# Optimization experiments

Hardware: AMD Instinct MI355X
Metric: run time of the kernel (lower is better)

## Reference

```python
import jax, jax.numpy as jnp
import numpy as np

N_HEADS = 16
ALIBI_BIAS_MAX = 8


def _alibi_bias(n_heads, seq_len):
    # MPT build_alibi_bias: bias[h, j] = -(seq_len-1-j) * slope_h, arranged [1,H,1,S]
    pos = jnp.arange(1 - seq_len, 1, dtype=jnp.float32).reshape(1, 1, 1, seq_len)
    m = jnp.arange(1, n_heads + 1, dtype=jnp.float32) * (ALIBI_BIAS_MAX / n_heads)
    slopes = (1.0 / jnp.exp2(m)).reshape(1, n_heads, 1, 1)
    return pos * slopes  # [1,H,1,S]


def setup_inputs() -> dict:
    key = jax.random.key(0)
    k1, k2, k3 = jax.random.split(key, 3)
    B, S, D = 1, 2048, 2048
    x = jax.random.normal(k1, (B, S, D), dtype=jnp.float32)
    # Wqkv: Linear(D, 3D, bias=False); out_proj: Linear(D, D, bias=False)
    w_qkv = jax.random.normal(k2, (3 * D, D), dtype=jnp.float32) * (1.0 / np.sqrt(D))
    w_out = jax.random.normal(k3, (D, D), dtype=jnp.float32) * (1.0 / np.sqrt(D))
    return {"x": x, "w_qkv": w_qkv, "w_out": w_out}


def reference(x, w_qkv, w_out):
    B, S, D = x.shape
    H = N_HEADS
    d = D // H
    qkv = x @ w_qkv.T                              # [B,S,3D]
    q, k, v = jnp.split(qkv, 3, axis=-1)
    q = q.reshape(B, S, H, d).transpose(0, 2, 1, 3)  # [B,H,S,d]
    k = k.reshape(B, S, H, d).transpose(0, 2, 1, 3)
    v = v.reshape(B, S, H, d).transpose(0, 2, 1, 3)
    scale = 1.0 / np.sqrt(d)
    scores = jnp.einsum('bhqd,bhkd->bhqk', q, k) * scale  # [B,H,S,S]
    scores = scores + _alibi_bias(H, S)
    min_val = jnp.finfo(scores.dtype).min
    causal = jnp.tril(jnp.ones((S, S), dtype=bool))
    scores = jnp.where(causal[None, None, :, :], scores, min_val)
    probs = jax.nn.softmax(scores.astype(jnp.float32), axis=-1).astype(q.dtype)
    out = jnp.einsum('bhqk,bhkd->bhqd', probs, v)  # [B,H,S,d]
    out = out.transpose(0, 2, 1, 3).reshape(B, S, D)
    return out @ w_out.T
```

## Files before the change

kernel.cpp:

```cpp
#include <hip/hip_runtime.h>

typedef __bf16 bf16;
typedef __bf16 bf16x8 __attribute__((ext_vector_type(8)));
typedef __bf16 bf16x4 __attribute__((ext_vector_type(4)));
typedef float f32x4 __attribute__((ext_vector_type(4)));

#if __has_builtin(__builtin_amdgcn_exp2f)
#define EXP2(x) __builtin_amdgcn_exp2f(x)
#else
#define EXP2(x) exp2f(x)
#endif

__device__ __forceinline__ void gload_lds16(const void* g, void* l) {
  __builtin_amdgcn_global_load_lds(
      (const __attribute__((address_space(1))) void*)g,
      (__attribute__((address_space(3))) void*)l, 16, 0, 0);
}

__global__ __launch_bounds__(256) void cast_all(const float* __restrict__ x,
                                                const float* __restrict__ wqkv,
                                                const float* __restrict__ wout,
                                                bf16* __restrict__ x_bf,
                                                bf16* __restrict__ wqkv_bf,
                                                bf16* __restrict__ wout_bf) {
  const int b = blockIdx.x;
  const float* src;
  bf16* dst;
  int i;
  if (b < 4096) {
    src = x; dst = x_bf; i = b * 1024 + threadIdx.x * 4;
  } else if (b < 16384) {
    src = wqkv; dst = wqkv_bf; i = (b - 4096) * 1024 + threadIdx.x * 4;
  } else {
    src = wout; dst = wout_bf; i = (b - 16384) * 1024 + threadIdx.x * 4;
  }
  float4 v = *(const float4*)(src + i);
  bf16x4 o = {(bf16)v.x, (bf16)v.y, (bf16)v.z, (bf16)v.w};
  *(bf16x4*)(dst + i) = o;
}

__global__ __launch_bounds__(512, 6) void gemm1_qkv(const bf16* __restrict__ A,
                                                    const bf16* __restrict__ B,
                                                    bf16* __restrict__ qb,
                                                    bf16* __restrict__ kb,
                                                    bf16* __restrict__ vt) {
  constexpr int K = 2048;
  __shared__ bf16 As[128 * 32];
  __shared__ bf16 Bs[128 * 32];
  const int t = threadIdx.x;
  const int w = t >> 6, l = t & 63;
  const int lr = l & 15, lg = l >> 4;
  const int nwg = 768;
  int lin = blockIdx.y * 48 + blockIdx.x;
  lin = (lin & 7) * (nwg >> 3) + (lin >> 3);
  const int bn = lin % 48;
  const int bm = lin / 48;
  const int wr = w >> 2, wc = w & 3;

  f32x4 acc[4][2] = {};
  const int row0 = t >> 2;
  const int cc0 = (t & 3) * 8;

  for (int k0 = 0; k0 < K; k0 += 32) {
    gload_lds16(A + (size_t)(bm * 128 + row0) * K + k0 + cc0, (char*)As + w * 1024);
    gload_lds16(B + (size_t)(bn * 128 + row0) * K + k0 + cc0, (char*)Bs + w * 1024);
    __syncthreads();
    bf16x8 af[4], bfr[2];
#pragma unroll
    for (int i = 0; i < 4; ++i)
      af[i] = *(const bf16x8*)((const char*)As + (wr * 64 + i * 16 + lr) * 64 + lg * 16);
#pragma unroll
    for (int j = 0; j < 2; ++j)
      bfr[j] = *(const bf16x8*)((const char*)Bs + (wc * 32 + j * 16 + lr) * 64 + lg * 16);
#pragma unroll
    for (int mi = 0; mi < 4; ++mi)
#pragma unroll
      for (int ni = 0; ni < 2; ++ni)
        acc[mi][ni] = __builtin_amdgcn_mfma_f32_16x16x32_bf16(af[mi], bfr[ni],
                                                              acc[mi][ni], 0, 0, 0);
    __syncthreads();
  }

  const int mb = bm * 128 + wr * 64 + lg * 4;
  const int nb = bn * 128 + wc * 32 + lr;
  if (bn * 128 < 4096) {
    bf16* dst = (bn * 128 < 2048) ? qb : kb;
#pragma unroll
    for (int mi = 0; mi < 4; ++mi) {
      const int mg = mb + mi * 16;
#pragma unroll
      for (int ni = 0; ni < 2; ++ni) {
        const int ng = (nb + ni * 16) & 2047;
#pragma unroll
        for (int rr = 0; rr < 4; ++rr)
          dst[(size_t)(mg + rr) * 2048 + ng] = (bf16)acc[mi][ni][rr];
      }
    }
  } else {
#pragma unroll
    for (int mi = 0; mi < 4; ++mi) {
      const int mg = mb + mi * 16;
#pragma unroll
      for (int ni = 0; ni < 2; ++ni) {
        const int dc = nb + ni * 16 - 4096;
        bf16x4 pk = {(bf16)acc[mi][ni][0], (bf16)acc[mi][ni][1],
                     (bf16)acc[mi][ni][2], (bf16)acc[mi][ni][3]};
        *(bf16x4*)(vt + (size_t)dc * 2048 + mg) = pk;
      }
    }
  }
}

__global__ __launch_bounds__(256) void gemm2_64x128(const bf16* __restrict__ A,
                                                    const bf16* __restrict__ B,
                                                    float* __restrict__ Cf) {
  constexpr int K = 2048, N = 2048;
  __shared__ bf16 As[64 * 32];
  __shared__ bf16 Bs[128 * 32];
  const int t = threadIdx.x;
  const int w = t >> 6, l = t & 63;
  const int lr = l & 15, lg = l >> 4;
  int lin = blockIdx.y * 16 + blockIdx.x;
  lin = (lin & 7) * 64 + (lin >> 3);
  const int bn = lin % 16;
  const int bm = lin / 16;

  f32x4 acc[4][2] = {};

  for (int k0 = 0; k0 < K; k0 += 32) {
    {
      const int row = t >> 2;
      gload_lds16(A + (size_t)(bm * 64 + row) * K + k0 + (t & 3) * 8,
                  (char*)As + (w * 64) * 16);
    }
#pragma unroll
    for (int r = 0; r < 2; ++r) {
      const int c = r * 256 + t;
      const int row = c >> 2;
      gload_lds16(B + (size_t)(bn * 128 + row) * K + k0 + (c & 3) * 8,
                  (char*)Bs + (r * 256 + w * 64) * 16);
    }
    __syncthreads();
    bf16x8 af[4], bfr[2];
#pragma unroll
    for (int i = 0; i < 4; ++i)
      af[i] = *(const bf16x8*)((const char*)As + (i * 16 + lr) * 64 + lg * 16);
#pragma unroll
    for (int i = 0; i < 2; ++i)
      bfr[i] = *(const bf16x8*)((const char*)Bs + (w * 32 + i * 16 + lr) * 64 + lg * 16);
#pragma unroll
    for (int mi = 0; mi < 4; ++mi)
#pragma unroll
      for (int ni = 0; ni < 2; ++ni)
        acc[mi][ni] = __builtin_amdgcn_mfma_f32_16x16x32_bf16(af[mi], bfr[ni],
                                                              acc[mi][ni], 0, 0, 0);
    __syncthreads();
  }

  const int mb = bm * 64 + lg * 4;
  const int nb = bn * 128 + w * 32 + lr;
#pragma unroll
  for (int mi = 0; mi < 4; ++mi) {
    const int mg = mb + mi * 16;
#pragma unroll
    for (int ni = 0; ni < 2; ++ni) {
      const int ng = nb + ni * 16;
#pragma unroll
      for (int rr = 0; rr < 4; ++rr)
        Cf[(size_t)(mg + rr) * N + ng] = acc[mi][ni][rr];
    }
  }
}

__global__ __launch_bounds__(256) void attn_kernel(const bf16* __restrict__ qb,
                                                   const bf16* __restrict__ kb,
                                                   const bf16* __restrict__ vt,
                                                   bf16* __restrict__ out,
                                                   bf16* __restrict__ pA,
                                                   bf16* __restrict__ pB,
                                                   float* __restrict__ ml) {
  constexpr int S = 2048, D = 2048;
  __shared__ bf16 Ks[64 * 128];
  __shared__ bf16 Vs[128 * 64];
  __shared__ bf16 Ps[4][16 * 64];
  const int t = threadIdx.x;
  const int w = t >> 6, l = t & 63;
  const int lr = l & 15, lg = l >> 4;
  const int b = blockIdx.x;

  int h, qt, piece, ns;
  if (b < 1024) {
    const int j = b >> 2;
    h = j & 15; qt = 16 + (j >> 4); piece = b & 3; ns = 4;
  } else if (b < 1280) {
    const int j = (b - 1024) >> 1;
    h = j & 15; qt = 8 + (j >> 4); piece = (b - 1024) & 1; ns = 2;
  } else {
    const int i = b - 1280;
    h = i & 15; qt = i >> 4; piece = 0; ns = 1;
  }
  const bool split = (ns > 1);
  const int q0 = qt * 64;
  const float slope2 = exp2f(-0.5f * (float)(h + 1)) * 1.4426950408889634f;
  const float scale2 = 0.08838834764831845f * 1.4426950408889634f;
  const int W = (int)(24.0f / slope2);
  const int s0 = (q0 > W) ? ((q0 - W) >> 6) : 0;
  const int len = qt + 1 - s0;
  const int start = s0 + (len * piece) / ns;
  const int end = s0 + (len * (piece + 1)) / ns;

  bf16x8 qf[4];
  {
    const bf16* qrow = qb + (size_t)(q0 + w * 16 + lr) * D + h * 128 + lg * 8;
#pragma unroll
    for (int kk = 0; kk < 4; ++kk) qf[kk] = *(const bf16x8*)(qrow + kk * 32);
  }

  f32x4 ob[8] = {};
  float mrow[4] = {-1e30f, -1e30f, -1e30f, -1e30f};
  float lrow[4] = {0.f, 0.f, 0.f, 0.f};

  auto stage = [&](int kv0) {
#pragma unroll
    for (int r = 0; r < 4; ++r) {
      {
        const int krow = r * 16 + (t >> 4);
        const int kcc = t & 15;
        gload_lds16(kb + (size_t)(kv0 + krow) * D + h * 128 + ((kcc ^ (krow & 7)) * 8),
                    (char*)Ks + (r * 256 + w * 64) * 16);
      }
      {
        const int vrow = r * 32 + (t >> 3);
        const int vcc = t & 7;
        gload_lds16(vt + (size_t)(h * 128 + vrow) * S + kv0 + ((vcc ^ (vrow & 7)) * 8),
                    (char*)Vs + (r * 256 + w * 64) * 16);
      }
    }
  };

  for (int tile = start; tile < end; ++tile) {
    const int kv0 = tile << 6;
    stage(kv0);
    __syncthreads();

    f32x4 sc[4] = {};
    __builtin_amdgcn_s_setprio(1);
#pragma unroll
    for (int jb = 0; jb < 4; ++jb) {
      const int row = jb * 16 + lr;
#pragma unroll
      for (int kk = 0; kk < 4; ++kk) {
        const int byte = row * 256 + ((kk * 64 + lg * 16) ^ ((row & 7) << 4));
        bf16x8 kf = *(const bf16x8*)((const char*)Ks + byte);
        sc[jb] = __builtin_amdgcn_mfma_f32_16x16x32_bf16(qf[kk], kf, sc[jb], 0, 0, 0);
      }
    }
    __builtin_amdgcn_s_setprio(0);

    float bias[4];
#pragma unroll
    for (int jb = 0; jb < 4; ++jb)
      bias[jb] = slope2 * (float)(kv0 + jb * 16 + lr - (S - 1));
    const bool diag = (tile == qt);
    float xv[4][4], m2r[4];
#pragma unroll
    for (int rr = 0; rr < 4; ++rr) {
#pragma unroll
      for (int jb = 0; jb < 4; ++jb) {
        float v = fmaf(sc[jb][rr], scale2, bias[jb]);
        if (diag && (jb * 16 + lr > w * 16 + lg * 4 + rr)) v = -1e30f;
        xv[rr][jb] = v;
      }
      float m2 = fmaxf(fmaxf(xv[rr][0], xv[rr][1]), fmaxf(xv[rr][2], xv[rr][3]));
      m2 = fmaxf(m2, __shfl_xor(m2, 1));
      m2 = fmaxf(m2, __shfl_xor(m2, 2));
      m2 = fmaxf(m2, __shfl_xor(m2, 4));
      m2 = fmaxf(m2, __shfl_xor(m2, 8));
      m2r[rr] = m2;
    }
    float need = fmaxf(fmaxf(m2r[0] - mrow[0], m2r[1] - mrow[1]),
                       fmaxf(m2r[2] - mrow[2], m2r[3] - mrow[3]));
    if (!__all(need <= 8.0f)) {
#pragma unroll
      for (int rr = 0; rr < 4; ++rr) {
        const float mnew = fmaxf(mrow[rr], m2r[rr]);
        const float cf = EXP2(mrow[rr] - mnew);
        lrow[rr] *= cf;
        mrow[rr] = mnew;
#pragma unroll
        for (int db = 0; db < 8; ++db) ob[db][rr] *= cf;
      }
    }
    char* pbase = (char*)Ps[w];
#pragma unroll
    for (int rr = 0; rr < 4; ++rr) {
      const int prow = lg * 4 + rr;
      const int sw = (prow & 7) << 4;
      float ps = 0.f;
#pragma unroll
      for (int jb = 0; jb < 4; ++jb) {
        const float p = EXP2(xv[rr][jb] - mrow[rr]);
        *(bf16*)(pbase + ((prow * 128 + jb * 32 + lr * 2) ^ sw)) = (bf16)p;
        ps += p;
      }
      lrow[rr] += ps;
    }

    bf16x8 pf[2];
#pragma unroll
    for (int s = 0; s < 2; ++s)
      pf[s] = *(const bf16x8*)(pbase + ((lr * 128 + s * 64 + lg * 16) ^ ((lr & 7) << 4)));
    __builtin_amdgcn_s_setprio(1);
#pragma unroll
    for (int db = 0; db < 8; ++db) {
      const int vrow = db * 16 + lr;
#pragma unroll
      for (int s = 0; s < 2; ++s) {
        const int byte = vrow * 128 + ((s * 64 + lg * 16) ^ ((vrow & 7) << 4));
        bf16x8 vf = *(const bf16x8*)((const char*)Vs + byte);
        ob[db] = __builtin_amdgcn_mfma_f32_16x16x32_bf16(pf[s], vf, ob[db], 0, 0, 0);
      }
    }
    __builtin_amdgcn_s_setprio(0);
    __syncthreads();
  }

  if (!split) {
#pragma unroll
    for (int rr = 0; rr < 4; ++rr) {
      float ls = lrow[rr];
      ls += __shfl_xor(ls, 1);
      ls += __shfl_xor(ls, 2);
      ls += __shfl_xor(ls, 4);
      ls += __shfl_xor(ls, 8);
      const float inv = 1.0f / ls;
      const int mg = q0 + w * 16 + lg * 4 + rr;
#pragma unroll
      for (int db = 0; db < 8; ++db)
        out[(size_t)mg * D + h * 128 + db * 16 + lr] = (bf16)(ob[db][rr] * inv);
    }
  } else {
    bf16* po = (b < 1024) ? pA + (size_t)b * 8192 : pB + (size_t)(b - 1024) * 8192;
#pragma unroll
    for (int rr = 0; rr < 4; ++rr) {
      float ls = lrow[rr];
      ls += __shfl_xor(ls, 1);
      ls += __shfl_xor(ls, 2);
      ls += __shfl_xor(ls, 4);
      ls += __shfl_xor(ls, 8);
      const int row = w * 16 + lg * 4 + rr;
#pragma unroll
      for (int db = 0; db < 8; ++db)
        po[row * 128 + db * 16 + lr] = (bf16)ob[db][rr];
      if (lr == 0) {
        ml[b * 128 + row] = mrow[rr];
        ml[b * 128 + 64 + row] = ls;
      }
    }
  }
}

__global__ __launch_bounds__(256) void attn_merge(const bf16* __restrict__ pA,
                                                  const bf16* __restrict__ pB,
                                                  const float* __restrict__ ml,
                                                  bf16* __restrict__ out) {
  const int j = blockIdx.x;
  const int t = threadIdx.x;
  int ns, c0, h, qt;
  if (j < 256) {
    ns = 4; c0 = 4 * j; h = j & 15; qt = 16 + (j >> 4);
  } else {
    const int j2 = j - 256;
    ns = 2; c0 = 1024 + 2 * j2; h = j2 & 15; qt = 8 + (j2 >> 4);
  }
  const int q0 = qt * 64;
  const int row = t >> 2;
  const int col0 = (t & 3) * 32;

  float m[4], lv[4];
  float M = -1e30f;
  for (int i = 0; i < ns; ++i) {
    m[i] = ml[(c0 + i) * 128 + row];
    lv[i] = ml[(c0 + i) * 128 + 64 + row];
    M = fmaxf(M, m[i]);
  }
  float wsum = 0.f, wgt[4];
  for (int i = 0; i < ns; ++i) {
    wgt[i] = EXP2(m[i] - M);
    wsum += wgt[i] * lv[i];
  }
  const float inv = 1.0f / wsum;

  float accv[32] = {};
  for (int i = 0; i < ns; ++i) {
    const int c = c0 + i;
    const bf16* po = (c < 1024) ? pA + (size_t)c * 8192 : pB + (size_t)(c - 1024) * 8192;
    const bf16* pr = po + row * 128 + col0;
    const float wi = wgt[i];
#pragma unroll
    for (int k = 0; k < 32; ++k) accv[k] += wi * (float)pr[k];
  }
  bf16* o = out + (size_t)(q0 + row) * 2048 + h * 128 + col0;
#pragma unroll
  for (int k = 0; k < 4; ++k) {
    bf16x8 o8;
#pragma unroll
    for (int e = 0; e < 8; ++e) o8[e] = (bf16)(accv[k * 8 + e] * inv);
    *(bf16x8*)(o + k * 8) = o8;
  }
}

extern "C" void kernel_launch(void* const* d_in, const int* in_sizes, int n_in,
                              void* d_out, int out_size, void* d_ws, size_t ws_size,
                              hipStream_t stream) {
  (void)in_sizes; (void)n_in; (void)out_size; (void)ws_size;
  const float* x = (const float*)d_in[0];
  const float* wqkv = (const float*)d_in[1];
  const float* wout = (const float*)d_in[2];
  float* out = (float*)d_out;

  bf16* x_bf = (bf16*)d_ws;
  bf16* wqkv_bf = x_bf + (size_t)2048 * 2048;
  bf16* wout_bf = wqkv_bf + (size_t)6144 * 2048;
  bf16* qb = wout_bf + (size_t)2048 * 2048;
  bf16* kb = qb + (size_t)2048 * 2048;
  bf16* vt = kb + (size_t)2048 * 2048;
  bf16* attn = wqkv_bf;
  bf16* pA = wqkv_bf + (size_t)2048 * 2048;
  bf16* pB = x_bf;
  float* ml = (float*)((char*)d_ws + (size_t)4 * 1024 * 1024);

  cast_all<<<20480, 256, 0, stream>>>(x, wqkv, wout, x_bf, wqkv_bf, wout_bf);
  gemm1_qkv<<<dim3(48, 16), 512, 0, stream>>>(x_bf, wqkv_bf, qb, kb, vt);
  attn_kernel<<<1408, 256, 0, stream>>>(qb, kb, vt, attn, pA, pB, ml);
  attn_merge<<<384, 256, 0, stream>>>(pA, pB, ml, attn);
  gemm2_64x128<<<dim3(16, 32), 256, 0, stream>>>(attn, wout_bf, out);
}
```

Before: 173.2 us.

## Rewrite QKV GEMM with 256x256 tiles, double-buffered swizzled LDS and interleaved prefetch

The QKV projection GEMM moves from 128x128 tiles with a K-step of 32 and a single LDS buffer to 256x256 tiles with a K-step of 64. It uses 128 KB of dynamic LDS, double-buffered with an XOR swizzle, and interleaves the next tile's global-to-LDS loads between quarter-tile MFMA groups, which are also raised in priority. The goal is more data reuse per byte loaded and hiding load latency behind the matrix math. The cost is only 192 workgroups, which underfills a 256-CU device, plus higher register and LDS pressure.

```diff
diff --git a/kernel.cpp b/kernel.cpp
--- a/kernel.cpp
+++ b/kernel.cpp
@@ -39,76 +39,127 @@
   *(bf16x4*)(dst + i) = o;
 }
 
-__global__ __launch_bounds__(512, 6) void gemm1_qkv(const bf16* __restrict__ A,
+__global__ __launch_bounds__(512, 2) void gemm1_qkv(const bf16* __restrict__ A,
                                                     const bf16* __restrict__ B,
                                                     bf16* __restrict__ qb,
                                                     bf16* __restrict__ kb,
                                                     bf16* __restrict__ vt) {
   constexpr int K = 2048;
-  __shared__ bf16 As[128 * 32];
-  __shared__ bf16 Bs[128 * 32];
+  extern __shared__ char smem[];
   const int t = threadIdx.x;
   const int w = t >> 6, l = t & 63;
   const int lr = l & 15, lg = l >> 4;
-  const int nwg = 768;
-  int lin = blockIdx.y * 48 + blockIdx.x;
-  lin = (lin & 7) * (nwg >> 3) + (lin >> 3);
-  const int bn = lin % 48;
-  const int bm = lin / 48;
   const int wr = w >> 2, wc = w & 3;
 
-  f32x4 acc[4][2] = {};
-  const int row0 = t >> 2;
-  const int cc0 = (t & 3) * 8;
-
-  for (int k0 = 0; k0 < K; k0 += 32) {
-    gload_lds16(A + (size_t)(bm * 128 + row0) * K + k0 + cc0, (char*)As + w * 1024);
-    gload_lds16(B + (size_t)(bn * 128 + row0) * K + k0 + cc0, (char*)Bs + w * 1024);
-    __syncthreads();
-    bf16x8 af[4], bfr[2];
-#pragma unroll
-    for (int i = 0; i < 4; ++i)
-      af[i] = *(const bf16x8*)((const char*)As + (wr * 64 + i * 16 + lr) * 64 + lg * 16);
-#pragma unroll
-    for (int j = 0; j < 2; ++j)
-      bfr[j] = *(const bf16x8*)((const char*)Bs + (wc * 32 + j * 16 + lr) * 64 + lg * 16);
-#pragma unroll
-    for (int mi = 0; mi < 4; ++mi)
-#pragma unroll
-      for (int ni = 0; ni < 2; ++ni)
-        acc[mi][ni] = __builtin_amdgcn_mfma_f32_16x16x32_bf16(af[mi], bfr[ni],
-                                                              acc[mi][ni], 0, 0, 0);
-    __syncthreads();
-  }
-
-  const int mb = bm * 128 + wr * 64 + lg * 4;
-  const int nb = bn * 128 + wc * 32 + lr;
-  if (bn * 128 < 4096) {
-    bf16* dst = (bn * 128 < 2048) ? qb : kb;
-#pragma unroll
-    for (int mi = 0; mi < 4; ++mi) {
-      const int mg = mb + mi * 16;
-#pragma unroll
-      for (int ni = 0; ni < 2; ++ni) {
-        const int ng = (nb + ni * 16) & 2047;
+  int lin = blockIdx.x;
+  lin = (lin & 7) * 24 + (lin >> 3);
+  const int bn = lin % 24, bm = lin / 24;
+  const int am0 = bm * 256, bn0 = bn * 256;
+
+  f32x4 acc[8][4] = {};
+
+  auto stageH = [&](const bf16* M, int lbase, int rowbase, int k0, int half, int b) {
+#pragma unroll
+    for (int r = 0; r < 2; ++r) {
+      const int u = r * 512 + t;
+      const int row = half * 128 + (u >> 3);
+      const int kc = u & 7;
+      gload_lds16(M + (size_t)(rowbase + row) * K + k0 + ((kc ^ (row & 7)) * 8),
+                  smem + lbase + b * 32768 + half * 16384 + (r * 512 + w * 64) * 16);
+    }
+  };
+
+#define AFRAG(MH, buf)                                                         \
+  _Pragma("unroll") for (int mi = 0; mi < 4; ++mi)                             \
+  _Pragma("unroll") for (int ks = 0; ks < 2; ++ks)                             \
+    a[mi * 2 + ks] = *(const bf16x8*)(                                         \
+        smem + (buf)*32768 +                                                   \
+        (wr * 128 + (MH)*64 + mi * 16 + lr) * 128 +                            \
+        (((ks * 4 + lg) ^ (lr & 7)) * 16));
+
+#define BFRAG(NH, buf, dst)                                                    \
+  _Pragma("unroll") for (int ni = 0; ni < 2; ++ni)                             \
+  _Pragma("unroll") for (int ks = 0; ks < 2; ++ks)                             \
+    dst[ni * 2 + ks] = *(const bf16x8*)(                                       \
+        smem + 65536 + (buf)*32768 +                                           \
+        (wc * 64 + (NH)*32 + ni * 16 + lr) * 128 +                             \
+        (((ks * 4 + lg) ^ (lr & 7)) * 16));
+
+#define QMFMA(MH, NH, bfr)                                                     \
+  __builtin_amdgcn_s_setprio(1);                                               \
+  _Pragma("unroll") for (int mi = 0; mi < 4; ++mi)                             \
+  _Pragma("unroll") for (int ni = 0; ni < 2; ++ni)                             \
+  _Pragma("unroll") for (int ks = 0; ks < 2; ++ks)                             \
+    acc[(MH)*4 + mi][(NH)*2 + ni] = __builtin_amdgcn_mfma_f32_16x16x32_bf16(   \
+        a[mi * 2 + ks], bfr[ni * 2 + ks], acc[(MH)*4 + mi][(NH)*2 + ni],       \
+        0, 0, 0);                                                              \
+  __builtin_amdgcn_s_setprio(0);
+
+#define BAR __builtin_amdgcn_s_barrier()
+#define VMCNT0 asm volatile("s_waitcnt vmcnt(0)" ::: "memory")
+
+  stageH(A, 0, am0, 0, 0, 0);
+  stageH(A, 0, am0, 0, 1, 0);
+  stageH(B, 65536, bn0, 0, 0, 0);
+  stageH(B, 65536, bn0, 0, 1, 0);
+  VMCNT0;
+  __syncthreads();
+
+  for (int tt = 0; tt < 32; ++tt) {
+    const int buf = tt & 1, nbf = buf ^ 1;
+    const int k0n = (tt + 1) * 64;
+    const bool pf = (tt < 31);
+    bf16x8 a[8], b0[4], b1[4];
+
+    AFRAG(0, buf);
+    BFRAG(0, buf, b0);
+    if (pf) stageH(A, 0, am0, k0n, 0, nbf);
+    BAR;
+    QMFMA(0, 0, b0);
+    BAR;
+    BFRAG(1, buf, b1);
+    if (pf) stageH(A, 0, am0, k0n, 1, nbf);
+    BAR;
+    QMFMA(0, 1, b1);
+    BAR;
+    AFRAG(1, buf);
+    if (pf) stageH(B, 65536, bn0, k0n, 0, nbf);
+    BAR;
+    QMFMA(1, 0, b0);
+    BAR;
+    if (pf) stageH(B, 65536, bn0, k0n, 1, nbf);
+    BAR;
+    QMFMA(1, 1, b1);
+    VMCNT0;
+    BAR;
+  }
+
+  const int mb = am0 + wr * 128 + lg * 4;
+  const int nb = bn0 + wc * 64 + lr;
+#pragma unroll
+  for (int m = 0; m < 8; ++m) {
+    const int mg = mb + m * 16;
+#pragma unroll
+    for (int j = 0; j < 4; ++j) {
+      const int ng = nb + j * 16;
+      if (ng < 4096) {
+        bf16* dst = (ng < 2048) ? qb : kb;
+        const int ngl = ng & 2047;
 #pragma unroll
         for (int rr = 0; rr < 4; ++rr)
-          dst[(size_t)(mg + rr) * 2048 + ng] = (bf16)acc[mi][ni][rr];
-      }
-    }
-  } else {
-#pragma unroll
-    for (int mi = 0; mi < 4; ++mi) {
-      const int mg = mb + mi * 16;
-#pragma unroll
-      for (int ni = 0; ni < 2; ++ni) {
-        const int dc = nb + ni * 16 - 4096;
-        bf16x4 pk = {(bf16)acc[mi][ni][0], (bf16)acc[mi][ni][1],
-                     (bf16)acc[mi][ni][2], (bf16)acc[mi][ni][3]};
-        *(bf16x4*)(vt + (size_t)dc * 2048 + mg) = pk;
-      }
-    }
-  }
+          dst[(size_t)(mg + rr) * 2048 + ngl] = (bf16)acc[m][j][rr];
+      } else {
+        bf16x4 pk = {(bf16)acc[m][j][0], (bf16)acc[m][j][1],
+                     (bf16)acc[m][j][2], (bf16)acc[m][j][3]};
+        *(bf16x4*)(vt + (size_t)(ng - 4096) * 2048 + mg) = pk;
+      }
+    }
+  }
+#undef AFRAG
+#undef BFRAG
+#undef QMFMA
+#undef BAR
+#undef VMCNT0
 }
 
 __global__ __launch_bounds__(256) void gemm2_64x128(const bf16* __restrict__ A,
@@ -430,8 +481,15 @@
   bf16* pB = x_bf;
   float* ml = (float*)((char*)d_ws + (size_t)4 * 1024 * 1024);
 
+  static int lds_ok = 0;
+  if (!lds_ok) {
+    (void)hipFuncSetAttribute((const void*)gemm1_qkv,
+                              hipFuncAttributeMaxDynamicSharedMemorySize, 131072);
+    lds_ok = 1;
+  }
+
   cast_all<<<20480, 256, 0, stream>>>(x, wqkv, wout, x_bf, wqkv_bf, wout_bf);
-  gemm1_qkv<<<dim3(48, 16), 512, 0, stream>>>(x_bf, wqkv_bf, qb, kb, vt);
+  gemm1_qkv<<<192, 512, 131072, stream>>>(x_bf, wqkv_bf, qb, kb, vt);
   attn_kernel<<<1408, 256, 0, stream>>>(qb, kb, vt, attn, pA, pB, ml);
   attn_merge<<<384, 256, 0, stream>>>(pA, pB, ml, attn);
   gemm2_64x128<<<dim3(16, 32), 256, 0, stream>>>(attn, wout_bf, out);
```

Measured after the change: 171.9 us. About the same (-0.8%).
